# Performance work log

Measured on AMD Instinct MI355X. Metric: run time of the kernel, lower is better.

Reference implementation:

```python
import jax, jax.numpy as jnp
import numpy as np

# Arbitrary non-contiguous kernel tap offsets (constructor arg sk_ind)
SK_IND = np.array([-512, -256, -128, -96, -64, -48, -32, -24, -16, -12, -8, -6,
                   -4, -3, -2, -1, 0, 1, 2, 3, 4, 6, 8, 12, 16, 24, 32, 48,
                   64, 96, 128, 256], dtype=np.int32)
IN_CHANNELS = 64
OUT_CHANNELS = 64
BATCH = 16
INPUT_LEN = 4096


def setup_inputs() -> dict:
    key = jax.random.key(0)
    k1, k2 = jax.random.split(key)
    x = jax.random.normal(k1, (BATCH, IN_CHANNELS, INPUT_LEN), dtype=jnp.float32)
    sk_weights = jax.random.normal(k2, (OUT_CHANNELS, IN_CHANNELS, SK_IND.shape[0]), dtype=jnp.float32)
    return {"x": x, "sk_weights": sk_weights}


def reference(x, sk_weights):
    # x: [B, Cin, L]; sk_weights: [Cout, Cin, K]
    B, C, L = x.shape
    low_pad = max(-int(SK_IND.min()), 0)   # zeros consumed by negative taps
    high_pad = max(int(SK_IND.max()), 0)   # zeros consumed by positive taps
    # Original pads zeros AFTER the signal: [x, zeros(high_pad), zeros(low_pad)];
    # negative numpy indices then wrap into the trailing low_pad zeros.
    padded = jnp.concatenate([x, jnp.zeros((B, C, high_pad + low_pad), x.dtype)], axis=-1)
    padded_len = L + high_pad + low_pad
    idx = SK_IND[:, None] + np.arange(L)                 # [K, L], static
    idx = np.where(idx < 0, padded_len + idx, idx)       # emulate numpy negative-index wrap
    gathered = padded[:, :, idx]                          # [B, Cin, K, L]
    # Per-position GEMM: contract over (Cin, K)
    return jnp.einsum('oik,bikl->bol', sk_weights, gathered)  # [B, Cout, L]
```

## Files before the change

### kernel.cpp

```cpp
#include <hip/hip_runtime.h>


#define B_    16
#define CIN   64
#define COUT  64
#define LEN   4096
#define PAD_LO 512
#define PAD_HI 256
#define LPAD  (LEN + PAD_LO + PAD_HI)
#define NTAP  32

typedef float f32x4 __attribute__((ext_vector_type(4)));
typedef short bf16x8_s __attribute__((ext_vector_type(8)));
typedef __bf16 bf16x8_b __attribute__((ext_vector_type(8)));
typedef unsigned short u16x8 __attribute__((ext_vector_type(8)));

template <typename V>
static __device__ inline auto mfma_16x16x32_bf16(V a, V b, f32x4 c, int)
    -> decltype(__builtin_amdgcn_mfma_f32_16x16x32_bf16(a, b, c, 0, 0, 0)) {
  return __builtin_amdgcn_mfma_f32_16x16x32_bf16(a, b, c, 0, 0, 0);
}
template <typename V>
static __device__ inline f32x4 mfma_16x16x32_bf16(V a, V b, f32x4 c, long) {
  return __builtin_amdgcn_mfma_f32_16x16x32_bf16(
      __builtin_bit_cast(bf16x8_b, a), __builtin_bit_cast(bf16x8_b, b), c, 0, 0, 0);
}

static __device__ inline unsigned short f32_to_bf16_rne(float f) {
  unsigned int u = __builtin_bit_cast(unsigned int, f);
  u += 0x7fffu + ((u >> 16) & 1u);
  return (unsigned short)(u >> 16);
}

static __device__ inline void async_copy16(const void* g, void* l) {
  __builtin_amdgcn_global_load_lds((const __attribute__((address_space(1))) unsigned int*)g,
                                   (__attribute__((address_space(3))) unsigned int*)l, 16, 0, 0);
}

__global__ __launch_bounds__(256) void prep_xw(const float* __restrict__ x,
                                               const float* __restrict__ w,
                                               unsigned short* __restrict__ xp,
                                               unsigned short* __restrict__ wf) {
  __shared__ float tile[64][65];
  const int b = blockIdx.y;
  const int lp0 = blockIdx.x * 64;
  const int tid = threadIdx.x;
  const bool data = (lp0 >= PAD_LO) && (lp0 < PAD_LO + LEN);
  if (data) {
    const int l0 = lp0 - PAD_LO;
#pragma unroll
    for (int it = 0; it < 4; ++it) {
      const int pidx = it * 256 + tid;
      const int il = pidx >> 4;
      const int lq = (pidx & 15) * 4;
      const float4 v = *(const float4*)&x[(size_t)(b * CIN + il) * LEN + l0 + lq];
      tile[lq + 0][il] = v.x;
      tile[lq + 1][il] = v.y;
      tile[lq + 2][il] = v.z;
      tile[lq + 3][il] = v.w;
    }
  } else if (lp0 < PAD_LO) {
    const int base = (b * 8 + blockIdx.x) * 1024;
#pragma unroll
    for (int it = 0; it < 4; ++it) {
      const int e = base + it * 256 + tid;
      const int j = e & 7;
      const int lane = (e >> 3) & 63;
      const int m = (e >> 9) & 3;
      const int c = (e >> 11) & 1;
      const int t = e >> 12;
      const int o = m * 16 + (lane & 15);
      const int i = c * 32 + (lane >> 4) * 8 + j;
      wf[e] = f32_to_bf16_rne(w[(size_t)(o * CIN + i) * NTAP + t]);
    }
  }
  __syncthreads();
#pragma unroll
  for (int it = 0; it < 2; ++it) {
    const int pidx = it * 256 + tid;
    const int ll = pidx >> 3;
    const int i8 = (pidx & 7) * 8;
    u16x8 v = {0, 0, 0, 0, 0, 0, 0, 0};
    if (data) {
#pragma unroll
      for (int j = 0; j < 8; ++j) v[j] = f32_to_bf16_rne(tile[ll][i8 + j]);
    }
    *(u16x8*)&xp[(size_t)(b * LPAD + lp0 + ll) * CIN + i8] = v;
  }
}

__global__ __launch_bounds__(512, 2) void sconv_main(const unsigned short* __restrict__ xp,
                                                     const unsigned short* __restrict__ wf,
                                                     float* __restrict__ out) {
  constexpr int TAP[NTAP] = {-512, -256, -128, -96, -64, -48, -32, -24, -16, -12, -8,
                             -6,   -4,   -3,   -2,  -1,  0,   1,   2,   3,   4,  6,
                             8,    12,   16,   24,  32,  48,  64,  96,  128, 256};
  __shared__ alignas(16) char smem[131072];

  const int id = blockIdx.x;
  const int b = (id & 7) * 2 + (id >> 7);
  const int l0 = ((id >> 3) & 15) * 256;
  const int lb = l0 + PAD_LO;
  const int tid = threadIdx.x;
  const int wv = tid >> 6, lane = tid & 63;
  const int q = lane >> 4, r = lane & 15;
  const int lh = wv >> 1, ch = wv & 1;

  const char* xbase = (const char*)xp + ((size_t)b * LPAD + lb) * (CIN * 2);
  const char* wbase = (const char*)wf;

  auto stageB = [&](int a0, int ng) {
    for (int g = wv; g < ng; g += 8) {
      const int ra = a0 + g * 8 + (lane >> 3);
      const int cs = (lane & 7) ^ (ra & 7);
      const int sb = (lb + a0 + g * 8) & 1023;
      async_copy16(xbase + (ptrdiff_t)ra * 128 + cs * 16, smem + sb * 128);
    }
  };

  bf16x8_s Wreg[2][4], Breg[2][4];
  f32x4 acc[4][4] = {};

  auto loadW = [&](int tt, int p) {
    const char* src = wbase + tt * 8192 + ch * 4096 + lane * 16;
#pragma unroll
    for (int m = 0; m < 4; ++m)
      Wreg[p][m] = *(const bf16x8_s*)(src + m * 1024);
  };
  auto readB = [&](int tt, int p) {
    const int e = (TAP[tt] + r) & 7;
#pragma unroll
    for (int n = 0; n < 4; ++n) {
      const int slot = (lb + TAP[tt] + lh * 64 + 16 * n + r) & 1023;
      Breg[p][n] = *(const bf16x8_s*)(smem + slot * 128 + (((ch * 4 + q) ^ e) << 4));
    }
  };

  loadW(0, 0);
  stageB(-512, 84);

#pragma unroll
  for (int g = 0; g < 8; ++g) {
    __syncthreads();
    readB(4 * g, 0);
    if (g < 7) {
      const int dstart = TAP[4 * g + 3] + 256;
      const int dend = TAP[4 * g + 7] + 256;
      const int a0 = dstart & ~7;
      stageB(a0, (dend - a0 + 7) >> 3);
    }
    __builtin_amdgcn_sched_barrier(0);
#pragma unroll
    for (int u = 0; u < 4; ++u) {
      const int t = 4 * g + u, p = t & 1;
      if (t + 1 < NTAP) {
        loadW(t + 1, p ^ 1);
        if ((t + 1) & 3) readB(t + 1, p ^ 1);
      }
      __builtin_amdgcn_sched_barrier(0);
#pragma unroll
      for (int m = 0; m < 4; ++m)
#pragma unroll
        for (int n = 0; n < 4; ++n)
          acc[m][n] = mfma_16x16x32_bf16(Wreg[p][m], Breg[p][n], acc[m][n], 0);
    }
  }

  __syncthreads();
  if (ch == 1) {
#pragma unroll
    for (int m = 0; m < 4; ++m)
#pragma unroll
      for (int n = 0; n < 4; ++n)
        *(f32x4*)(smem + lh * 16384 + ((m * 4 + n) * 64 + lane) * 16) = acc[m][n];
  }
  __syncthreads();
  if (ch == 0) {
#pragma unroll
    for (int m = 0; m < 4; ++m)
#pragma unroll
      for (int n = 0; n < 4; ++n) {
        const f32x4 other = *(const f32x4*)(smem + lh * 16384 + ((m * 4 + n) * 64 + lane) * 16);
        const f32x4 v = acc[m][n] + other;
#pragma unroll
        for (int d = 0; d < 4; ++d) {
          const int o = 16 * m + 4 * q + d;
          const int l = l0 + lh * 64 + 16 * n + r;
          out[((size_t)b * COUT + o) * LEN + l] = v[d];
        }
      }
  }
}

extern "C" void kernel_launch(void* const* d_in, const int* in_sizes, int n_in,
                              void* d_out, int out_size, void* d_ws, size_t ws_size,
                              hipStream_t stream) {
  const float* x = (const float*)d_in[0];
  const float* w = (const float*)d_in[1];
  float* out = (float*)d_out;

  unsigned short* xp = (unsigned short*)d_ws;
  unsigned short* wfp = xp + (size_t)B_ * LPAD * CIN;

  prep_xw<<<dim3(LPAD / 64, B_), 256, 0, stream>>>(x, w, xp, wfp);
  sconv_main<<<dim3(256), 512, 0, stream>>>(xp, wfp, out);
}
```

Baseline: 90.04 us.

## Halve main-kernel tile to 128 positions and stage input per tap

The main conv kernel now runs 512 blocks of 256 threads, each covering 128 output positions, with a 64KB LDS ring buffer in place of 128KB. Input staging moves from once per 4-tap group to every tap, with a barrier per tap and a single B register buffer. This is meant to raise occupancy and parallelism and to cut LDS footprint. In exchange it adds more barriers, re-reads weights per block, and gives up the register prefetch of B.

```diff
diff --git a/kernel.cpp b/kernel.cpp
--- a/kernel.cpp
+++ b/kernel.cpp
@@ -89,17 +89,17 @@
   }
 }
 
-__global__ __launch_bounds__(512, 2) void sconv_main(const unsigned short* __restrict__ xp,
+__global__ __launch_bounds__(256, 2) void sconv_main(const unsigned short* __restrict__ xp,
                                                      const unsigned short* __restrict__ wf,
                                                      float* __restrict__ out) {
   constexpr int TAP[NTAP] = {-512, -256, -128, -96, -64, -48, -32, -24, -16, -12, -8,
                              -6,   -4,   -3,   -2,  -1,  0,   1,   2,   3,   4,  6,
                              8,    12,   16,   24,  32,  48,  64,  96,  128, 256};
-  __shared__ alignas(16) char smem[131072];
+  __shared__ alignas(16) char smem[65536];
 
   const int id = blockIdx.x;
-  const int b = (id & 7) * 2 + (id >> 7);
-  const int l0 = ((id >> 3) & 15) * 256;
+  const int b = (id & 7) * 2 + (id >> 8);
+  const int l0 = ((id >> 3) & 31) * 128;
   const int lb = l0 + PAD_LO;
   const int tid = threadIdx.x;
   const int wv = tid >> 6, lane = tid & 63;
@@ -110,15 +110,15 @@
   const char* wbase = (const char*)wf;
 
   auto stageB = [&](int a0, int ng) {
-    for (int g = wv; g < ng; g += 8) {
+    for (int g = wv; g < ng; g += 4) {
       const int ra = a0 + g * 8 + (lane >> 3);
       const int cs = (lane & 7) ^ (ra & 7);
-      const int sb = (lb + a0 + g * 8) & 1023;
+      const int sb = (lb + a0 + g * 8) & 511;
       async_copy16(xbase + (ptrdiff_t)ra * 128 + cs * 16, smem + sb * 128);
     }
   };
 
-  bf16x8_s Wreg[2][4], Breg[2][4];
+  bf16x8_s Wreg[2][4], Breg[4];
   f32x4 acc[4][4] = {};
 
   auto loadW = [&](int tt, int p) {
@@ -127,43 +127,36 @@
     for (int m = 0; m < 4; ++m)
       Wreg[p][m] = *(const bf16x8_s*)(src + m * 1024);
   };
-  auto readB = [&](int tt, int p) {
+  auto readB = [&](int tt) {
     const int e = (TAP[tt] + r) & 7;
 #pragma unroll
     for (int n = 0; n < 4; ++n) {
-      const int slot = (lb + TAP[tt] + lh * 64 + 16 * n + r) & 1023;
-      Breg[p][n] = *(const bf16x8_s*)(smem + slot * 128 + (((ch * 4 + q) ^ e) << 4));
+      const int slot = (lb + TAP[tt] + lh * 64 + 16 * n + r) & 511;
+      Breg[n] = *(const bf16x8_s*)(smem + slot * 128 + (((ch * 4 + q) ^ e) << 4));
     }
   };
 
   loadW(0, 0);
-  stageB(-512, 84);
-
-#pragma unroll
-  for (int g = 0; g < 8; ++g) {
+  stageB(TAP[0], 16);
+
+#pragma unroll
+  for (int t = 0; t < NTAP; ++t) {
+    const int p = t & 1;
     __syncthreads();
-    readB(4 * g, 0);
-    if (g < 7) {
-      const int dstart = TAP[4 * g + 3] + 256;
-      const int dend = TAP[4 * g + 7] + 256;
-      const int a0 = dstart & ~7;
-      stageB(a0, (dend - a0 + 7) >> 3);
+    readB(t);
+    if (t + 1 < NTAP) {
+      const int lo = (TAP[t] + 128 > TAP[t + 1]) ? (TAP[t] + 128) : TAP[t + 1];
+      const int a0 = lo & ~7;
+      const int ng = (TAP[t + 1] + 128 - a0 + 7) >> 3;
+      stageB(a0, ng);
+      loadW(t + 1, p ^ 1);
     }
     __builtin_amdgcn_sched_barrier(0);
 #pragma unroll
-    for (int u = 0; u < 4; ++u) {
-      const int t = 4 * g + u, p = t & 1;
-      if (t + 1 < NTAP) {
-        loadW(t + 1, p ^ 1);
-        if ((t + 1) & 3) readB(t + 1, p ^ 1);
-      }
-      __builtin_amdgcn_sched_barrier(0);
-#pragma unroll
-      for (int m = 0; m < 4; ++m)
-#pragma unroll
-        for (int n = 0; n < 4; ++n)
-          acc[m][n] = mfma_16x16x32_bf16(Wreg[p][m], Breg[p][n], acc[m][n], 0);
-    }
+    for (int m = 0; m < 4; ++m)
+#pragma unroll
+      for (int n = 0; n < 4; ++n)
+        acc[m][n] = mfma_16x16x32_bf16(Wreg[p][m], Breg[n], acc[m][n], 0);
   }
 
   __syncthreads();
@@ -203,5 +196,5 @@
   unsigned short* wfp = xp + (size_t)B_ * LPAD * CIN;
 
   prep_xw<<<dim3(LPAD / 64, B_), 256, 0, stream>>>(x, w, xp, wfp);
-  sconv_main<<<dim3(256), 512, 0, stream>>>(xp, wfp, out);
-}
+  sconv_main<<<dim3(512), 256, 0, stream>>>(xp, wfp, out);
+}
```

Result: slower. 94.70 us (+5.2%).

## Stage full input window to LDS upfront and remap prep grid to 1D

Applied to the files above, without the earlier changes.

The main kernel now copies the whole 1024-row halo window into the LDS ring in one prologue, with a single barrier, instead of streaming it in eight groups with a barrier per group. The tap loop is flattened to a simple double-buffered loop with no further barriers or async copies. The prep kernel uses a 1D grid whose block-to-batch mapping interleaves batches, likely to match the main kernel's placement. In exchange, the initial load latency is fully exposed before any MFMA work starts, and staging no longer overlaps compute.

```diff
diff --git a/kernel.cpp b/kernel.cpp
--- a/kernel.cpp
+++ b/kernel.cpp
@@ -42,8 +42,10 @@
                                                unsigned short* __restrict__ xp,
                                                unsigned short* __restrict__ wf) {
   __shared__ float tile[64][65];
-  const int b = blockIdx.y;
-  const int lp0 = blockIdx.x * 64;
+  const int id = blockIdx.x;
+  const int b = 2 * (id & 7) + ((id >> 3) & 1);
+  const int xt = id >> 4;
+  const int lp0 = xt * 64;
   const int tid = threadIdx.x;
   const bool data = (lp0 >= PAD_LO) && (lp0 < PAD_LO + LEN);
   if (data) {
@@ -60,7 +62,7 @@
       tile[lq + 3][il] = v.w;
     }
   } else if (lp0 < PAD_LO) {
-    const int base = (b * 8 + blockIdx.x) * 1024;
+    const int base = (b * 8 + xt) * 1024;
 #pragma unroll
     for (int it = 0; it < 4; ++it) {
       const int e = base + it * 256 + tid;
@@ -109,15 +111,6 @@
   const char* xbase = (const char*)xp + ((size_t)b * LPAD + lb) * (CIN * 2);
   const char* wbase = (const char*)wf;
 
-  auto stageB = [&](int a0, int ng) {
-    for (int g = wv; g < ng; g += 8) {
-      const int ra = a0 + g * 8 + (lane >> 3);
-      const int cs = (lane & 7) ^ (ra & 7);
-      const int sb = (lb + a0 + g * 8) & 1023;
-      async_copy16(xbase + (ptrdiff_t)ra * 128 + cs * 16, smem + sb * 128);
-    }
-  };
-
   bf16x8_s Wreg[2][4], Breg[2][4];
   f32x4 acc[4][4] = {};
 
@@ -136,34 +129,31 @@
     }
   };
 
+#pragma unroll
+  for (int i = 0; i < 16; ++i) {
+    const int g = wv + i * 8;
+    const int ra = -512 + g * 8 + (lane >> 3);
+    const int cs = (lane & 7) ^ (ra & 7);
+    const int sb = (lb - 512 + g * 8) & 1023;
+    async_copy16(xbase + (ptrdiff_t)ra * 128 + cs * 16, smem + sb * 128);
+  }
   loadW(0, 0);
-  stageB(-512, 84);
+  __syncthreads();
+  readB(0, 0);
 
 #pragma unroll
-  for (int g = 0; g < 8; ++g) {
-    __syncthreads();
-    readB(4 * g, 0);
-    if (g < 7) {
-      const int dstart = TAP[4 * g + 3] + 256;
-      const int dend = TAP[4 * g + 7] + 256;
-      const int a0 = dstart & ~7;
-      stageB(a0, (dend - a0 + 7) >> 3);
+  for (int t = 0; t < NTAP; ++t) {
+    const int p = t & 1;
+    if (t + 1 < NTAP) {
+      loadW(t + 1, p ^ 1);
+      readB(t + 1, p ^ 1);
     }
     __builtin_amdgcn_sched_barrier(0);
 #pragma unroll
-    for (int u = 0; u < 4; ++u) {
-      const int t = 4 * g + u, p = t & 1;
-      if (t + 1 < NTAP) {
-        loadW(t + 1, p ^ 1);
-        if ((t + 1) & 3) readB(t + 1, p ^ 1);
-      }
-      __builtin_amdgcn_sched_barrier(0);
+    for (int m = 0; m < 4; ++m)
 #pragma unroll
-      for (int m = 0; m < 4; ++m)
-#pragma unroll
-        for (int n = 0; n < 4; ++n)
-          acc[m][n] = mfma_16x16x32_bf16(Wreg[p][m], Breg[p][n], acc[m][n], 0);
-    }
+      for (int n = 0; n < 4; ++n)
+        acc[m][n] = mfma_16x16x32_bf16(Wreg[p][m], Breg[p][n], acc[m][n], 0);
   }
 
   __syncthreads();
@@ -202,6 +192,6 @@
   unsigned short* xp = (unsigned short*)d_ws;
   unsigned short* wfp = xp + (size_t)B_ * LPAD * CIN;
 
-  prep_xw<<<dim3(LPAD / 64, B_), 256, 0, stream>>>(x, w, xp, wfp);
+  prep_xw<<<dim3((LPAD / 64) * B_), 256, 0, stream>>>(x, w, xp, wfp);
   sconv_main<<<dim3(256), 512, 0, stream>>>(xp, wfp, out);
 }
```

Result: no change. 88.93 us (-1.2%).
